# Performance work log

Hardware: AMD Instinct MI355X
Metric: run time of the kernel (lower is better)

Reference implementation:

```python
import jax, jax.numpy as jnp
import numpy as np
import math

B, S, D, H = 2, 2048, 1024, 16
D_K = D // H


def setup_inputs() -> dict:
    key = jax.random.key(0)
    ks = jax.random.split(key, 9)
    scale = 0.02
    return {
        "query": jax.random.normal(ks[0], (B, S, D), dtype=jnp.float32),
        "key": jax.random.normal(ks[1], (B, S, D), dtype=jnp.float32),
        "value": jax.random.normal(ks[2], (B, S, D), dtype=jnp.float32),
        "padding_mask": jax.random.bernoulli(ks[3], 0.1, (B, 1, 1, S)),
        "Wq": jax.random.normal(ks[4], (D, D), dtype=jnp.float32) * scale,
        "bq": jnp.zeros((D,), dtype=jnp.float32),
        "Wk": jax.random.normal(ks[5], (D, D), dtype=jnp.float32) * scale,
        "bk": jnp.zeros((D,), dtype=jnp.float32),
        "Wv": jax.random.normal(ks[6], (D, D), dtype=jnp.float32) * scale,
        "bv": jnp.zeros((D,), dtype=jnp.float32),
        "Wo": jax.random.normal(ks[7], (D, D), dtype=jnp.float32) * scale,
        "bo": jnp.zeros((D,), dtype=jnp.float32),
    }


def reference(query, key, value, padding_mask, Wq, bq, Wk, bk, Wv, bv, Wo, bo):
    # projections -> [B, H, S, d_k]
    q = (query @ Wq + bq).reshape(B, S, H, D_K).transpose(0, 2, 1, 3)
    k = (key @ Wk + bk).reshape(B, S, H, D_K).transpose(0, 2, 1, 3)
    v = (value @ Wv + bv).reshape(B, S, H, D_K).transpose(0, 2, 1, 3)

    # scores: [B, H, S, S]
    scores = jnp.einsum("bhqd,bhkd->bhqk", q, k) / math.sqrt(D_K)

    # faithful to original: triu(scores, 1).bool() -> True where upper-tri score != 0,
    # masked positions get value 1e-10 (NOT -inf) before softmax
    causal_mask = jnp.triu(scores, k=1) != 0
    scores = jnp.where(causal_mask, jnp.float32(1e-10), scores)
    scores = jnp.where(padding_mask, jnp.float32(1e-10), scores)

    attn = jax.nn.softmax(scores, axis=-1)
    out = jnp.einsum("bhqk,bhkd->bhqd", attn, v)  # [B, H, S, d_k]
    out = out.transpose(0, 2, 1, 3).reshape(B, S, D)
    return out @ Wo + bo
```

## Files before the change

kernel.cpp:

```cpp
#include <hip/hip_runtime.h>
#include <hip/hip_bf16.h>
#include <cstdint>
#include <cstddef>

typedef __hip_bfloat16 bf16;
typedef __attribute__((ext_vector_type(8))) short short8;
typedef __attribute__((ext_vector_type(4))) short s4v;
typedef __attribute__((ext_vector_type(4))) float floatx4;

#define B_ 2
#define S_ 2048
#define D_ 1024
#define H_ 16
#define DK_ 64
#define M_ 4096
#define HEADELEMS 131072
#define TILEELEMS 4096
#define QSCALE 0.1803368801111204f

struct __align__(8) bf16x4 { bf16 x, y, z, w; };

__device__ __forceinline__ floatx4 mfma16(short8 a, short8 b, floatx4 c) {
  return __builtin_amdgcn_mfma_f32_16x16x32_bf16(a, b, c, 0, 0, 0);
}
__device__ __forceinline__ void gl_lds16(const bf16* g, bf16* l) {
  __builtin_amdgcn_global_load_lds((const __attribute__((address_space(1))) void*)g,
                                   (__attribute__((address_space(3))) void*)l, 16, 0, 0);
}
__device__ __forceinline__ float bs2f(short s) {
  bf16 b = *reinterpret_cast<bf16*>(&s);
  return __bfloat162float(b);
}
__device__ __forceinline__ s4v pack4(float p0, float p1, float p2, float p3) {
  union { __hip_bfloat162 h; short2 s; } ua, ub;
  ua.h = __float22bfloat162_rn(make_float2(p0, p1));
  ub.h = __float22bfloat162_rn(make_float2(p2, p3));
  s4v r = {ua.s.x, ua.s.y, ub.s.x, ub.s.y};
  return r;
}
__device__ __forceinline__ float fast_exp2(float x) {
#if __has_builtin(__builtin_amdgcn_exp2f)
  return __builtin_amdgcn_exp2f(x);
#else
  float r; asm("v_exp_f32 %0, %1" : "=v"(r) : "v"(x)); return r;
#endif
}

__global__ void prep_kernel(const float* __restrict__ q_in, const float* __restrict__ k_in,
                            const float* __restrict__ v_in,
                            const float* __restrict__ Wq, const float* __restrict__ Wk,
                            const float* __restrict__ Wv, const float* __restrict__ Wo,
                            bf16* __restrict__ xq, bf16* __restrict__ xk, bf16* __restrict__ xv,
                            bf16* __restrict__ wqt, bf16* __restrict__ wkt,
                            bf16* __restrict__ wvt, bf16* __restrict__ wot,
                            const unsigned int* __restrict__ pmask, int* __restrict__ flag) {
  __shared__ bf16 tile[64][66];
  __shared__ int sbyte;
  const int blk = blockIdx.x;
  const int tid = threadIdx.x;
  if (blk < 12288) {
    const int z = blk >> 12;
    const int i = ((blk & 4095) << 8) | tid;
    const float* src = (z == 0) ? q_in : (z == 1) ? k_in : v_in;
    bf16* dst = (z == 0) ? xq : (z == 1) ? xk : xv;
    float4 v = ((const float4*)src)[i];
    bf16x4 o = { __float2bfloat16(v.x), __float2bfloat16(v.y),
                 __float2bfloat16(v.z), __float2bfloat16(v.w) };
    ((bf16x4*)dst)[i] = o;
  } else if (blk < 13312) {
    const int t = blk - 12288;
    const int z = t >> 8;
    const int rc = t & 255;
    const int r0 = (rc >> 4) * 64, c0 = (rc & 15) * 64;
    const float* src = (z == 0) ? Wq : (z == 1) ? Wk : (z == 2) ? Wv : Wo;
    bf16* dst = (z == 0) ? wqt : (z == 1) ? wkt : (z == 2) ? wvt : wot;
    const int lr = tid >> 4;
    const int lc4 = (tid & 15) * 4;
#pragma unroll
    for (int i = 0; i < 4; ++i) {
      const int r = lr + i * 16;
      float4 v = *(const float4*)(src + (size_t)(r0 + r) * D_ + c0 + lc4);
      tile[r][lc4 + 0] = __float2bfloat16(v.x);
      tile[r][lc4 + 1] = __float2bfloat16(v.y);
      tile[r][lc4 + 2] = __float2bfloat16(v.z);
      tile[r][lc4 + 3] = __float2bfloat16(v.w);
    }
    __syncthreads();
    const int orr = tid & 63;
    const int oc0 = tid >> 6;
#pragma unroll
    for (int j = 0; j < 16; ++j) {
      const int oc = oc0 + j * 4;
      dst[(size_t)(c0 + oc) * D_ + r0 + orr] = tile[orr][oc];
    }
  } else {
    if (tid == 0) sbyte = 0;
    __syncthreads();
    for (int i = tid; i < (B_ * S_) / 4; i += 256) {
      const unsigned int v = pmask[i];
      if (((v & 0xFEFEFEFEu) == 0u) && ((v & 0xFFFFFF00u) != 0u)) sbyte = 1;
    }
    __syncthreads();
    if (tid == 0) *flag = sbyte;
  }
}

template<int MT>
__global__ __launch_bounds__(256, 2) void gemm_k(
    const bf16* __restrict__ A0, const bf16* __restrict__ A1, const bf16* __restrict__ A2,
    const bf16* __restrict__ W0, const bf16* __restrict__ W1, const bf16* __restrict__ W2,
    const float* __restrict__ b0, const float* __restrict__ b1, const float* __restrict__ b2,
    void* __restrict__ O0, void* __restrict__ O1, void* __restrict__ O2,
    const int mode01, const int Kd, const float sc)
{
  __shared__ __align__(16) bf16 sh[(MT + 128) * 32];
  bf16* As = sh;
  bf16* Bs = sh + MT * 32;
  const int z = blockIdx.z;
  const bf16* A = (z == 0) ? A0 : (z == 1) ? A1 : A2;
  const bf16* W = (z == 0) ? W0 : (z == 1) ? W1 : W2;
  const float* bias = (z == 0) ? b0 : (z == 1) ? b1 : b2;
  void* Cout = (z == 0) ? O0 : (z == 1) ? O1 : O2;
  const int mode = (z == 2) ? 1 : mode01;
  const float scz = (z == 0) ? sc : 1.f;

  constexpr int MI = MT / 32;
  const int tid = threadIdx.x;
  const int wave = tid >> 6, lane = tid & 63;
  const int quad = lane >> 4, lc = lane & 15;
  const int wm = (wave >> 1) * (MT / 2), wn = (wave & 1) * 64;
  const int m0 = blockIdx.y * MT, n0 = blockIdx.x * 128;

  const floatx4 zero4 = {0.f, 0.f, 0.f, 0.f};
  floatx4 acc[MI][4];
#pragma unroll
  for (int mi = 0; mi < MI; ++mi)
#pragma unroll
    for (int ni = 0; ni < 4; ++ni) acc[mi][ni] = zero4;

  const int ldr = lane >> 2;
  const int ldc = (lane & 3) * 8;
  const bf16* Ag = A + (size_t)(m0 + wave * (MT / 4) + ldr) * Kd + ldc;
  const bf16* Bg = W + (size_t)(n0 + wave * 32 + ldr) * Kd + ldc;
  bf16* As0 = As + wave * (MT / 4) * 32;
  bf16* Bs0 = Bs + wave * 32 * 32;

  for (int k0 = 0; k0 < Kd; k0 += 32) {
    gl_lds16(Ag + k0, As0);
    if (MT == 128) gl_lds16(Ag + k0 + (size_t)16 * Kd, As0 + 16 * 32);
    gl_lds16(Bg + k0, Bs0);
    gl_lds16(Bg + k0 + (size_t)16 * Kd, Bs0 + 16 * 32);
    __syncthreads();

    short8 af[MI], bfr[4];
#pragma unroll
    for (int i = 0; i < MI; ++i)
      af[i] = *(const short8*)(As + (wm + i * 16 + lc) * 32 + quad * 8);
#pragma unroll
    for (int i = 0; i < 4; ++i)
      bfr[i] = *(const short8*)(Bs + (wn + i * 16 + lc) * 32 + quad * 8);
#pragma unroll
    for (int mi = 0; mi < MI; ++mi)
#pragma unroll
      for (int ni = 0; ni < 4; ++ni)
        acc[mi][ni] = mfma16(af[mi], bfr[ni], acc[mi][ni]);
    __syncthreads();
  }

  if (mode == 2) {
    float* out = (float*)Cout;
#pragma unroll
    for (int mi = 0; mi < MI; ++mi)
#pragma unroll
      for (int ni = 0; ni < 4; ++ni) {
        const int col = n0 + wn + ni * 16 + lc;
        const float bv = bias[col];
        const int rbase = m0 + wm + mi * 16 + quad * 4;
#pragma unroll
        for (int r = 0; r < 4; ++r)
          out[(size_t)(rbase + r) * D_ + col] = acc[mi][ni][r] + bv;
      }
  } else {
    bf16* pool = sh + wave * 2048;
    float bvs[4];
#pragma unroll
    for (int ni = 0; ni < 4; ++ni) bvs[ni] = bias[n0 + wn + ni * 16 + lc];
    const int hcol = (n0 + wn) >> 6;
    const int mglob = m0 + wm;
    bf16* outb = (bf16*)Cout + (size_t)((mglob >> 11) * H_ + hcol) * HEADELEMS
               + (size_t)((mglob & (S_ - 1)) >> 6) * TILEELEMS;
#pragma unroll
    for (int half = 0; half < MI / 2; ++half) {
#pragma unroll
      for (int mi2 = 0; mi2 < 2; ++mi2) {
        const int mi = half * 2 + mi2;
#pragma unroll
        for (int ni = 0; ni < 4; ++ni) {
          const int dkl = ni * 16 + lc;
#pragma unroll
          for (int r = 0; r < 4; ++r) {
            const float v = (acc[mi][ni][r] + bvs[ni]) * scz;
            int idx;
            if (mode == 0) {
              const int c = (mi2 * 2 + (dkl >> 5)) * 64 + ((dkl >> 3) & 3) * 16 + quad * 4 + r;
              idx = c * 8 + (dkl & 7);
            } else {
              const int c = (mi2 * 4 + (dkl >> 4)) * 64 + quad * 16 + (dkl & 15);
              idx = c * 4 + r;
            }
            pool[idx] = __float2bfloat16(v);
          }
        }
      }
#pragma unroll
      for (int t = 0; t < 4; ++t) {
        const short8 vv = *(const short8*)(pool + t * 512 + lane * 8);
        *(short8*)(outb + half * 2048 + t * 512 + lane * 8) = vv;
      }
    }
  }
}

__global__ void suf_kernel(const bf16* __restrict__ vp, float* __restrict__ suf) {
  __shared__ float ts[32 * 64];
  const int bhid = blockIdx.x;
  const bf16* vb = vp + (size_t)bhid * HEADELEMS;
  const int tid = threadIdx.x;
  const int dk = tid & 63, g = tid >> 6;
  const int dkt = dk >> 4, lck = dk & 15;
  for (int T = g * 8; T < g * 8 + 8; ++T) {
    float sum = 0.f;
#pragma unroll
    for (int w = 0; w < 4; ++w)
#pragma unroll
      for (int qd = 0; qd < 4; ++qd) {
        const s4v x = *(const s4v*)(vb + (size_t)T * TILEELEMS
                                    + (size_t)(((w * 4 + dkt) * 64 + qd * 16 + lck)) * 4);
        sum += bs2f(x[0]) + bs2f(x[1]) + bs2f(x[2]) + bs2f(x[3]);
      }
    ts[T * 64 + dk] = sum;
  }
  __syncthreads();
  if (g == 0) {
    float run = 0.f;
    float* out = suf + (size_t)bhid * (33 * 64);
    out[32 * 64 + dk] = 0.f;
    for (int T = 31; T >= 0; --T) { run += ts[T * 64 + dk]; out[T * 64 + dk] = run; }
  }
}

template<bool DIAGP>
__device__ __forceinline__ void qk_tile(const short8 ak0, const short8 ak1,
                                        const short8 (&qf)[4][2],
                                        const unsigned int (&pmb)[4], const int T,
                                        float (&lacc)[4], s4v (&pf)[4],
                                        const int w, const int quad, const int lc,
                                        const bool diag) {
  const floatx4 z4 = {0.f, 0.f, 0.f, 0.f};
  const short ONE = (short)0x3F80;
#pragma unroll
  for (int qt = 0; qt < 4; ++qt) {
    if (DIAGP && diag && w > qt) {
      s4v o1 = {ONE, ONE, ONE, ONE};
      pf[qt] = o1;
      lacc[qt] += 4.f;
      continue;
    }
    floatx4 s = mfma16(ak0, qf[qt][0], z4);
    s = mfma16(ak1, qf[qt][1], s);
    float pv[4];
#pragma unroll
    for (int r = 0; r < 4; ++r) {
      bool m = ((pmb[r] >> T) & 1u) != 0u;
      if (DIAGP && diag && w == qt) m = m || (quad * 4 + r > lc);
      pv[r] = fast_exp2(m ? 0.f : s[r]);
      lacc[qt] += pv[r];
    }
    pf[qt] = pack4(pv[0], pv[1], pv[2], pv[3]);
  }
}

__device__ __forceinline__ void pv_step(const s4v (&va0)[4], const s4v (&va1)[4],
                                        const s4v (&pf0)[4], const s4v (&pf1)[4],
                                        floatx4 (&oacc)[4][4]) {
  short8 pB[4];
#pragma unroll
  for (int qt = 0; qt < 4; ++qt)
    pB[qt] = __builtin_shufflevector(pf0[qt], pf1[qt], 0, 1, 2, 3, 4, 5, 6, 7);
#pragma unroll
  for (int dkt = 0; dkt < 4; ++dkt) {
    const short8 av = __builtin_shufflevector(va0[dkt], va1[dkt], 0, 1, 2, 3, 4, 5, 6, 7);
#pragma unroll
    for (int qt = 0; qt < 4; ++qt)
      oacc[dkt][qt] = mfma16(av, pB[qt], oacc[dkt][qt]);
  }
}

__device__ __forceinline__ void stage8(const bf16* kb, const bf16* vb, bf16* slot,
                                       const int T0, const int T1,
                                       const int wl, const int wreg) {
  const bf16* k0 = kb + (size_t)T0 * TILEELEMS + wl;
  const bf16* k1 = kb + (size_t)T1 * TILEELEMS + wl;
  const bf16* v0 = vb + (size_t)T0 * TILEELEMS + wl;
  const bf16* v1 = vb + (size_t)T1 * TILEELEMS + wl;
  gl_lds16(k0,       slot + wreg);
  gl_lds16(k0 + 512, slot + wreg + 512);
  gl_lds16(k1,       slot + 4096 + wreg);
  gl_lds16(k1 + 512, slot + 4096 + wreg + 512);
  gl_lds16(v0,       slot + 8192 + wreg);
  gl_lds16(v0 + 512, slot + 8192 + wreg + 512);
  gl_lds16(v1,       slot + 12288 + wreg);
  gl_lds16(v1 + 512, slot + 12288 + wreg + 512);
}

__global__ __launch_bounds__(256, 1) void attn_kernel(
    const bf16* __restrict__ qp, const bf16* __restrict__ kp,
    const bf16* __restrict__ vp, const float* __restrict__ suf,
    const void* __restrict__ pad, const int* __restrict__ flag,
    bf16* __restrict__ oa)
{
  __shared__ __align__(16) bf16 lds[32768];

  const int lin = blockIdx.x;
  const int xcd = lin & 7;
  const int t = lin >> 3;
  const int grp = t >> 4;
  const int jq = t & 15;
  const int bh = xcd + 8 * grp;
  const int b = bh >> 4, h = bh & 15;

  const int tid = threadIdx.x;
  const int w = tid >> 6, lane = tid & 63, quad = lane >> 4, lc = lane & 15;
  const int bytemode = *flag;

  const int wreg = w * 1024;
  const int wl = wreg + lane * 8;
  const int vl = wreg + lane * 4;

  const bf16* kb = kp + (size_t)bh * HEADELEMS;
  const bf16* vb = vp + (size_t)bh * HEADELEMS;

  unsigned int pmb[4] = {0u, 0u, 0u, 0u};
  if (bytemode) {
    const unsigned char* pp = (const unsigned char*)pad + b * S_ + w * 16 + quad * 4;
#pragma unroll
    for (int T = 0; T < 32; ++T) {
      const uchar4 u = *(const uchar4*)(pp + T * 64);
      pmb[0] |= (u.x ? 1u : 0u) << T;
      pmb[1] |= (u.y ? 1u : 0u) << T;
      pmb[2] |= (u.z ? 1u : 0u) << T;
      pmb[3] |= (u.w ? 1u : 0u) << T;
    }
  } else {
    const int* pp = (const int*)pad + b * S_ + w * 16 + quad * 4;
#pragma unroll
    for (int T = 0; T < 32; ++T) {
      const int4 u = *(const int4*)(pp + (size_t)T * 64);
      pmb[0] |= (u.x ? 1u : 0u) << T;
      pmb[1] |= (u.y ? 1u : 0u) << T;
      pmb[2] |= (u.z ? 1u : 0u) << T;
      pmb[3] |= (u.w ? 1u : 0u) << T;
    }
  }

#pragma unroll 1
  for (int qsel = 0; qsel < 2; ++qsel) {
    const int myqt = qsel ? jq : 31 - jq;
    const int mynt = myqt + 1;
    const int np = (mynt + 1) >> 1;

    const bf16* qb = qp + (size_t)bh * HEADELEMS + (size_t)myqt * TILEELEMS;
    gl_lds16(qb + wl,       lds + 16384 + wreg);
    gl_lds16(qb + wl + 512, lds + 16384 + wreg + 512);
    stage8(kb, vb, lds, 0, 1, wl, wreg);
    asm volatile("s_waitcnt vmcnt(0)" ::: "memory");
    __syncthreads();

    short8 qf[4][2];
#pragma unroll
    for (int qt = 0; qt < 4; ++qt)
#pragma unroll
      for (int hh = 0; hh < 2; ++hh)
        qf[qt][hh] = *(const short8*)(lds + 16384 + qt * 1024 + hh * 512 + lane * 8);
    __syncthreads();

    const floatx4 zero4 = {0.f, 0.f, 0.f, 0.f};
    floatx4 oacc[4][4];
#pragma unroll
    for (int i = 0; i < 4; ++i)
#pragma unroll
      for (int jj = 0; jj < 4; ++jj) oacc[i][jj] = zero4;
    float lacc[4] = {0.f, 0.f, 0.f, 0.f};

#pragma unroll 1
    for (int p = 0; p < np; ++p) {
      if (p + 1 < np) {
        stage8(kb, vb, lds + (((p + 1) & 1) << 14), 2 * p + 2, 2 * p + 3, wl, wreg);
        asm volatile("s_waitcnt vmcnt(8)" ::: "memory");
      } else {
        asm volatile("s_waitcnt vmcnt(0)" ::: "memory");
      }
      __builtin_amdgcn_sched_barrier(0);

      bf16* slot = lds + ((p & 1) << 14);
      const short8 ak00 = *(const short8*)(slot + wl);
      const short8 ak01 = *(const short8*)(slot + wl + 512);
      const short8 ak10 = *(const short8*)(slot + 4096 + wl);
      const short8 ak11 = *(const short8*)(slot + 4096 + wl + 512);
      s4v va0[4], va1[4];
#pragma unroll
      for (int dkt = 0; dkt < 4; ++dkt) {
        va0[dkt] = *(const s4v*)(slot + 8192 + vl + dkt * 256);
        va1[dkt] = *(const s4v*)(slot + 12288 + vl + dkt * 256);
      }

      const int T0 = 2 * p, T1 = 2 * p + 1;
      s4v pf0[4], pf1[4];
      if (p + 1 < np) {
        qk_tile<false>(ak00, ak01, qf, pmb, T0, lacc, pf0, w, quad, lc, false);
        qk_tile<false>(ak10, ak11, qf, pmb, T1, lacc, pf1, w, quad, lc, false);
      } else {
        qk_tile<true>(ak00, ak01, qf, pmb, T0, lacc, pf0, w, quad, lc, T0 == mynt - 1);
        if (T1 < mynt) {
          qk_tile<true>(ak10, ak11, qf, pmb, T1, lacc, pf1, w, quad, lc, true);
        } else {
          const s4v zz = {0, 0, 0, 0};
#pragma unroll
          for (int qt = 0; qt < 4; ++qt) pf1[qt] = zz;
        }
      }
      pv_step(va0, va1, pf0, pf1, oacc);
    }

    __syncthreads();

    float* fbuf = (float*)lds;
    bf16* obuf = lds + 8704;
    float* lbuf = (float*)(lds + 13312);

#pragma unroll
    for (int qt = 0; qt < 4; ++qt) {
      float v = lacc[qt];
      v += __shfl_xor(v, 16);
      v += __shfl_xor(v, 32);
      if (quad == 0) lbuf[w * 64 + qt * 16 + lc] = v;
    }
    __syncthreads();
    float ls = lbuf[0 * 64 + w * 16 + lc] + lbuf[1 * 64 + w * 16 + lc]
             + lbuf[2 * 64 + w * 16 + lc] + lbuf[3 * 64 + w * 16 + lc];
    ls += (float)(S_ - mynt * 64);
    const float linv = 1.f / ls;
    const float* sufp = suf + (size_t)bh * (33 * 64) + mynt * 64;

#pragma unroll
    for (int dktG = 0; dktG < 4; ++dktG) {
#pragma unroll
      for (int qt = 0; qt < 4; ++qt) {
        const floatx4 a = oacc[dktG][qt];
        float* dst = fbuf + (w * 4 + qt) * 272 + lc;
#pragma unroll
        for (int r = 0; r < 4; ++r) dst[(quad * 4 + r) * 17] = a[r];
      }
      __syncthreads();
      const float4 sv4 = *(const float4*)(sufp + dktG * 16 + quad * 4);
      float v[4];
#pragma unroll
      for (int r = 0; r < 4; ++r) {
        const int e = (quad * 4 + r) * 17 + lc;
        v[r] = fbuf[(0 * 4 + w) * 272 + e] + fbuf[(1 * 4 + w) * 272 + e]
             + fbuf[(2 * 4 + w) * 272 + e] + fbuf[(3 * 4 + w) * 272 + e];
      }
      v[0] = (v[0] + sv4.x) * linv; v[1] = (v[1] + sv4.y) * linv;
      v[2] = (v[2] + sv4.z) * linv; v[3] = (v[3] + sv4.w) * linv;
      bf16x4 pk = { __float2bfloat16(v[0]), __float2bfloat16(v[1]),
                    __float2bfloat16(v[2]), __float2bfloat16(v[3]) };
      *(bf16x4*)(obuf + (w * 16 + lc) * 72 + dktG * 16 + quad * 4) = pk;
      __syncthreads();
    }

    const size_t obase = (size_t)(b * S_ + myqt * 64) * D_ + h * 64;
#pragma unroll
    for (int it = 0; it < 2; ++it) {
      const int idx = it * 256 + tid;
      const int row = idx >> 3, c8 = (idx & 7) * 8;
      const short8 vv = *(const short8*)(obuf + row * 72 + c8);
      *(short8*)(oa + obase + (size_t)row * D_ + c8) = vv;
    }
    __syncthreads();
  }
}

extern "C" void kernel_launch(void* const* d_in, const int* in_sizes, int n_in,
                              void* d_out, int out_size, void* d_ws, size_t ws_size,
                              hipStream_t stream) {
  (void)in_sizes; (void)n_in; (void)out_size; (void)ws_size;
  const float* q_in = (const float*)d_in[0];
  const float* k_in = (const float*)d_in[1];
  const float* v_in = (const float*)d_in[2];
  const void*  pmask = d_in[3];
  const float* Wq = (const float*)d_in[4];
  const float* bq = (const float*)d_in[5];
  const float* Wk = (const float*)d_in[6];
  const float* bk = (const float*)d_in[7];
  const float* Wv = (const float*)d_in[8];
  const float* bv = (const float*)d_in[9];
  const float* Wo = (const float*)d_in[10];
  const float* bo = (const float*)d_in[11];

  char* ws = (char*)d_ws;
  bf16* xq  = (bf16*)(ws + 0);
  bf16* xk  = (bf16*)(ws + 8388608);
  bf16* xv  = (bf16*)(ws + 16777216);
  bf16* wqt = (bf16*)(ws + 25165824);
  bf16* wkt = (bf16*)(ws + 27262976);
  bf16* wvt = (bf16*)(ws + 29360128);
  bf16* wot = (bf16*)(ws + 31457280);
  bf16* qpp = (bf16*)(ws + 33554432);
  bf16* kpp = (bf16*)(ws + 41943040);
  bf16* vpp = (bf16*)(ws + 50331648);
  float* suf = (float*)(ws + 25165824);
  int*  flg = (int*)(ws + 58720256);
  bf16* oa  = xq;

  prep_kernel<<<13313, 256, 0, stream>>>(q_in, k_in, v_in, Wq, Wk, Wv, Wo,
                                         xq, xk, xv, wqt, wkt, wvt, wot,
                                         (const unsigned int*)pmask, flg);

  gemm_k<128><<<dim3(8, 32, 3), 256, 0, stream>>>(xq, xk, xv, wqt, wkt, wvt,
                                                  bq, bk, bv, qpp, kpp, vpp, 0, D_, QSCALE);
  suf_kernel<<<32, 256, 0, stream>>>(vpp, suf);

  attn_kernel<<<512, 256, 0, stream>>>(qpp, kpp, vpp, suf, pmask, flg, oa);

  gemm_k<64><<<dim3(8, 64, 1), 256, 0, stream>>>(oa, oa, oa, wot, wot, wot,
                                                 bo, bo, bo, d_out, d_out, d_out, 2, D_, 1.f);
}
```

Baseline: 222.7 us.

## Double-buffer GEMM LDS tiles with K=64 stages and XOR swizzle

Rewrites the GEMM main loop to prefetch the next K=64 tile into a second LDS buffer while computing on the current one, replacing the single-buffer K=32 loop that had two barriers per step. LDS rows are XOR-swizzled to avoid bank conflicts, the grid is transposed so blocks sharing a weight tile run together, and the output projection switches from a 64-row to a 128-row tile. This roughly quadruples LDS use, which may lower occupancy. The larger output tile also halves that GEMM's block count.

Measured after the change: 216.3 us. -2.9%, faster.

```diff
diff --git a/kernel.cpp b/kernel.cpp
--- a/kernel.cpp
+++ b/kernel.cpp
@@ -113,9 +113,8 @@
     void* __restrict__ O0, void* __restrict__ O1, void* __restrict__ O2,
     const int mode01, const int Kd, const float sc)
 {
-  __shared__ __align__(16) bf16 sh[(MT + 128) * 32];
-  bf16* As = sh;
-  bf16* Bs = sh + MT * 32;
+  constexpr int ROWS = MT + 128;
+  __shared__ __align__(16) bf16 sh[2 * ROWS * 64];
   const int z = blockIdx.z;
   const bf16* A = (z == 0) ? A0 : (z == 1) ? A1 : A2;
   const bf16* W = (z == 0) ? W0 : (z == 1) ? W1 : W2;
@@ -129,7 +128,7 @@
   const int wave = tid >> 6, lane = tid & 63;
   const int quad = lane >> 4, lc = lane & 15;
   const int wm = (wave >> 1) * (MT / 2), wn = (wave & 1) * 64;
-  const int m0 = blockIdx.y * MT, n0 = blockIdx.x * 128;
+  const int m0 = blockIdx.x * MT, n0 = blockIdx.y * 128;
 
   const floatx4 zero4 = {0.f, 0.f, 0.f, 0.f};
   floatx4 acc[MI][4];
@@ -138,33 +137,57 @@
 #pragma unroll
     for (int ni = 0; ni < 4; ++ni) acc[mi][ni] = zero4;
 
-  const int ldr = lane >> 2;
-  const int ldc = (lane & 3) * 8;
-  const bf16* Ag = A + (size_t)(m0 + wave * (MT / 4) + ldr) * Kd + ldc;
-  const bf16* Bg = W + (size_t)(n0 + wave * 32 + ldr) * Kd + ldc;
-  bf16* As0 = As + wave * (MT / 4) * 32;
-  bf16* Bs0 = Bs + wave * 32 * 32;
-
-  for (int k0 = 0; k0 < Kd; k0 += 32) {
-    gl_lds16(Ag + k0, As0);
-    if (MT == 128) gl_lds16(Ag + k0 + (size_t)16 * Kd, As0 + 16 * 32);
-    gl_lds16(Bg + k0, Bs0);
-    gl_lds16(Bg + k0 + (size_t)16 * Kd, Bs0 + 16 * 32);
-    __syncthreads();
-
-    short8 af[MI], bfr[4];
-#pragma unroll
-    for (int i = 0; i < MI; ++i)
-      af[i] = *(const short8*)(As + (wm + i * 16 + lc) * 32 + quad * 8);
-#pragma unroll
-    for (int i = 0; i < 4; ++i)
-      bfr[i] = *(const short8*)(Bs + (wn + i * 16 + lc) * 32 + quad * 8);
-#pragma unroll
-    for (int mi = 0; mi < MI; ++mi)
-#pragma unroll
-      for (int ni = 0; ni < 4; ++ni)
-        acc[mi][ni] = mfma16(af[mi], bfr[ni], acc[mi][ni]);
-    __syncthreads();
+  const int srow = lane >> 3;
+  const int schunk = ((lane & 7) ^ srow) * 8;
+  const bf16* Ag = A + (size_t)(m0 + wave * (MT / 4) + srow) * Kd + schunk;
+  const bf16* Bg = W + (size_t)(n0 + wave * 32 + srow) * Kd + schunk;
+
+  auto stage = [&](bf16* buf, int k0) {
+    bf16* As0 = buf + wave * (MT / 4) * 64;
+    bf16* Bs0 = buf + MT * 64 + wave * 32 * 64;
+#pragma unroll
+    for (int j = 0; j < MT / 32; ++j)
+      gl_lds16(Ag + k0 + (size_t)(j * 8) * Kd, As0 + j * 512);
+#pragma unroll
+    for (int j = 0; j < 4; ++j)
+      gl_lds16(Bg + k0 + (size_t)(j * 8) * Kd, Bs0 + j * 512);
+  };
+
+  stage(sh, 0);
+  asm volatile("s_waitcnt vmcnt(0)" ::: "memory");
+  __syncthreads();
+
+  int cur = 0;
+  for (int k0 = 0; k0 < Kd; k0 += 64) {
+    bf16* cbuf = cur ? sh + ROWS * 64 : sh;
+    bf16* nbuf = cur ? sh : sh + ROWS * 64;
+    const bool more = (k0 + 64 < Kd);
+    if (more) stage(nbuf, k0 + 64);
+
+    const bf16* Ar = cbuf;
+    const bf16* Br = cbuf + MT * 64;
+    short8 af[2][MI], bfr[2][4];
+#pragma unroll
+    for (int kk = 0; kk < 2; ++kk) {
+#pragma unroll
+      for (int i = 0; i < MI; ++i)
+        af[kk][i] = *(const short8*)(Ar + (wm + i * 16 + lc) * 64
+                                     + (((kk * 4 + quad) ^ (lc & 7)) * 8));
+#pragma unroll
+      for (int i = 0; i < 4; ++i)
+        bfr[kk][i] = *(const short8*)(Br + (wn + i * 16 + lc) * 64
+                                      + (((kk * 4 + quad) ^ (lc & 7)) * 8));
+    }
+#pragma unroll
+    for (int kk = 0; kk < 2; ++kk)
+#pragma unroll
+      for (int mi = 0; mi < MI; ++mi)
+#pragma unroll
+        for (int ni = 0; ni < 4; ++ni)
+          acc[mi][ni] = mfma16(af[kk][mi], bfr[kk][ni], acc[mi][ni]);
+
+    __syncthreads();
+    cur ^= 1;
   }
 
   if (mode == 2) {
@@ -526,12 +549,12 @@
                                          xq, xk, xv, wqt, wkt, wvt, wot,
                                          (const unsigned int*)pmask, flg);
 
-  gemm_k<128><<<dim3(8, 32, 3), 256, 0, stream>>>(xq, xk, xv, wqt, wkt, wvt,
+  gemm_k<128><<<dim3(32, 8, 3), 256, 0, stream>>>(xq, xk, xv, wqt, wkt, wvt,
                                                   bq, bk, bv, qpp, kpp, vpp, 0, D_, QSCALE);
   suf_kernel<<<32, 256, 0, stream>>>(vpp, suf);
 
   attn_kernel<<<512, 256, 0, stream>>>(qpp, kpp, vpp, suf, pmask, flg, oa);
 
-  gemm_k<64><<<dim3(8, 64, 1), 256, 0, stream>>>(oa, oa, oa, wot, wot, wot,
-                                                 bo, bo, bo, d_out, d_out, d_out, 2, D_, 1.f);
-}
+  gemm_k<128><<<dim3(32, 8, 1), 256, 0, stream>>>(oa, oa, oa, wot, wot, wot,
+                                                  bo, bo, bo, d_out, d_out, d_out, 2, D_, 1.f);
+}
```
